# Optimization experiments

Measured on AMD Instinct MI355X. Metric: run time of the kernel, lower is better.

Reference implementation:

```python
import jax, jax.numpy as jnp
import numpy as np

EMD = 768
HEADS = 8
HEAD_DIM = EMD // HEADS


def setup_inputs() -> dict:
    key = jax.random.key(0)
    ks = jax.random.split(key, 9)
    s = 0.02
    x = jax.random.normal(ks[0], (4, 2048, EMD), dtype=jnp.float32)
    # torch nn.Linear weights: (out_features, in_features)
    Wq = jax.random.normal(ks[1], (EMD, EMD), dtype=jnp.float32) * s
    bq = jnp.zeros((EMD,), dtype=jnp.float32)
    Wk = jax.random.normal(ks[2], (EMD, EMD), dtype=jnp.float32) * s
    bk = jnp.zeros((EMD,), dtype=jnp.float32)
    Wv = jax.random.normal(ks[3], (EMD, EMD), dtype=jnp.float32) * s
    bv = jnp.zeros((EMD,), dtype=jnp.float32)
    Wo = jax.random.normal(ks[4], (EMD, EMD), dtype=jnp.float32) * s
    bo = jnp.zeros((EMD,), dtype=jnp.float32)
    return {"x": x, "Wq": Wq, "bq": bq, "Wk": Wk, "bk": bk,
            "Wv": Wv, "bv": bv, "Wo": Wo, "bo": bo}


def _split_heads(t):
    # [b, n, emd] -> [b, h, n, d]
    b, n, _ = t.shape
    return t.reshape(b, n, HEADS, HEAD_DIM).transpose(0, 2, 1, 3)


def reference(x, Wq, bq, Wk, bk, Wv, bv, Wo, bo):
    q = _split_heads(x @ Wq.T + bq)  # [b,h,n,d]
    k = _split_heads(x @ Wk.T + bk)
    v = _split_heads(x @ Wv.T + bv)
    energy = jnp.einsum('bhqd,bhkd->bhqk', q, k)  # [b,h,n,n]
    # NOTE: the original module applies softmax over the HEADS axis (dim=1),
    # then divides by sqrt(emd_size). We replicate that exactly.
    scaling = jnp.asarray(EMD ** 0.5, dtype=energy.dtype)
    attention = jax.nn.softmax(energy, axis=1) / scaling
    out = jnp.einsum('bhqk,bhkd->bhqd', attention, v)  # [b,h,n,d]
    b, h, n, d = out.shape
    out = out.transpose(0, 2, 1, 3).reshape(b, n, h * d)  # [b,n,emd]
    return out @ Wo.T + bo
```

## Files before the change

kernel.cpp:

```cpp
#include <hip/hip_runtime.h>
#include <stdint.h>

typedef __bf16 bf16;
typedef __bf16 bf16x4 __attribute__((ext_vector_type(4)));
typedef __bf16 bf16x8 __attribute__((ext_vector_type(8)));
typedef float  fx4    __attribute__((ext_vector_type(4)));

#define MFMA16(a, b, c) __builtin_amdgcn_mfma_f32_16x16x32_bf16((a), (b), (c), 0, 0, 0)


__device__ __forceinline__ void barrier_nodrain() {
  __asm__ __volatile__("" ::: "memory");
  __builtin_amdgcn_s_waitcnt(0xC07F);
  __builtin_amdgcn_s_barrier();
  __asm__ __volatile__("" ::: "memory");
}

__device__ __forceinline__ void wait_vm6() {
  __asm__ __volatile__("" ::: "memory");
  __builtin_amdgcn_s_waitcnt(0x0F76);
  __asm__ __volatile__("" ::: "memory");
}
__device__ __forceinline__ void wait_lgkm0() {
  __asm__ __volatile__("" ::: "memory");
  __builtin_amdgcn_s_waitcnt(0xC07F);
  __asm__ __volatile__("" ::: "memory");
}

__device__ __forceinline__ void gload_lds16(const void* g, void* l) {
  __builtin_amdgcn_global_load_lds(
      (const __attribute__((address_space(1))) void*)g,
      (__attribute__((address_space(3))) void*)l, 16, 0, 0);
}

__global__ __launch_bounds__(256)
void cvt_x_kernel(const float* __restrict__ x, bf16* __restrict__ xb) {
  const int i = (blockIdx.x * 256 + threadIdx.x) * 4;
  float4 v = *(const float4*)&x[i];
  bf16x4 o;
  o[0] = (bf16)v.x; o[1] = (bf16)v.y; o[2] = (bf16)v.z; o[3] = (bf16)v.w;
  *(bf16x4*)&xb[i] = o;
}

__global__ __launch_bounds__(256)
void gemm_qkv(const bf16* __restrict__ A,
              const float* __restrict__ Wq, const float* __restrict__ Wk,
              const float* __restrict__ Wv,
              const float* __restrict__ bq, const float* __restrict__ bk,
              const float* __restrict__ bv,
              bf16* __restrict__ Qo, bf16* __restrict__ Ka,
              bf16* __restrict__ Va) {
  constexpr int K = 768;
  __shared__ __align__(16) bf16 As[2][128 * 32];
  __shared__ __align__(16) bf16 Bs[128 * 32];

  const int tid  = threadIdx.x;
  const int wave = tid >> 6;
  const int lane = tid & 63;
  const int l15  = lane & 15;
  const int q4   = lane >> 4;
  const int wr   = wave >> 1;
  const int wc   = wave & 1;
  const int sel  = blockIdx.x / 6;
  const int cb0  = (blockIdx.x % 6) * 128;
  const int rb0  = blockIdx.y * 128;

  const float* W   = (sel == 0) ? Wq : (sel == 1) ? Wk : Wv;
  const float* bia = (sel == 0) ? bq : (sel == 1) ? bk : bv;

  const int ar0 = tid >> 2,         akc0 = (tid & 3) << 3;
  const int ar1 = ar0 + 64,         akc1 = akc0;

  fx4 acc[4][4];
#pragma unroll
  for (int i = 0; i < 4; i++)
#pragma unroll
    for (int j = 0; j < 4; j++) acc[i][j] = (fx4){0.f, 0.f, 0.f, 0.f};

  gload_lds16(&A[(size_t)(rb0 + ar0) * K + akc0], &As[0][wave * 512]);
  gload_lds16(&A[(size_t)(rb0 + ar1) * K + akc1], &As[0][(wave + 4) * 512]);

  int cur = 0;
  for (int k0 = 0; k0 < K; k0 += 32, cur ^= 1) {
    const float* wp0 = W + (size_t)(cb0 + ar0) * K + k0 + akc0;
    const float* wp1 = W + (size_t)(cb0 + ar1) * K + k0 + akc1;
    const float4 b0a = *(const float4*)wp0;
    const float4 b0b = *(const float4*)(wp0 + 4);
    const float4 b1a = *(const float4*)wp1;
    const float4 b1b = *(const float4*)(wp1 + 4);
    __asm__ __volatile__("" ::: "memory");

    const int kn = (k0 + 32 < K) ? k0 + 32 : k0;
    gload_lds16(&A[(size_t)(rb0 + ar0) * K + kn + akc0],
                &As[cur ^ 1][wave * 512]);
    gload_lds16(&A[(size_t)(rb0 + ar1) * K + kn + akc1],
                &As[cur ^ 1][(wave + 4) * 512]);
    __asm__ __volatile__("" ::: "memory");

    bf16x8 pb0, pb1;
    pb0[0] = (bf16)b0a.x; pb0[1] = (bf16)b0a.y;
    pb0[2] = (bf16)b0a.z; pb0[3] = (bf16)b0a.w;
    pb0[4] = (bf16)b0b.x; pb0[5] = (bf16)b0b.y;
    pb0[6] = (bf16)b0b.z; pb0[7] = (bf16)b0b.w;
    pb1[0] = (bf16)b1a.x; pb1[1] = (bf16)b1a.y;
    pb1[2] = (bf16)b1a.z; pb1[3] = (bf16)b1a.w;
    pb1[4] = (bf16)b1b.x; pb1[5] = (bf16)b1b.y;
    pb1[6] = (bf16)b1b.z; pb1[7] = (bf16)b1b.w;
    *(bf16x8*)&Bs[ar0 * 32 + akc0] = pb0;
    *(bf16x8*)&Bs[ar1 * 32 + akc1] = pb1;

    barrier_nodrain();

    bf16x8 a[4], b[4];
#pragma unroll
    for (int i = 0; i < 4; i++)
      a[i] = *(const bf16x8*)&As[cur][(wr * 64 + i * 16 + l15) * 32 + q4 * 8];
#pragma unroll
    for (int j = 0; j < 4; j++)
      b[j] = *(const bf16x8*)&Bs[(wc * 64 + j * 16 + l15) * 32 + q4 * 8];
#pragma unroll
    for (int i = 0; i < 4; i++)
#pragma unroll
      for (int j = 0; j < 4; j++)
        acc[i][j] = MFMA16(a[i], b[j], acc[i][j]);

    barrier_nodrain();
  }

  const int cb = cb0 + wc * 64;
  const int rb = rb0 + wr * 64;
#pragma unroll
  for (int j = 0; j < 4; j++) {
    const int o  = cb + j * 16 + l15;
    const float bj = bia[o];
    const int hh = o / 96;
    const int dd = o - hh * 96;
#pragma unroll
    for (int i = 0; i < 4; i++) {
      const int r0 = rb + i * 16 + q4 * 4;
      if (sel == 2) {
        const int bb = r0 >> 11;
        const int n2 = r0 & 2047;
        const size_t flat =
            ((size_t)((bb * 8 + hh) * 64 + (n2 >> 5))) * 3072 +
            ((n2 >> 3) & 3) * 768 + dd * 8 + (n2 & 7);
        bf16x4 pk;
#pragma unroll
        for (int r = 0; r < 4; r++) pk[r] = (bf16)(acc[i][j][r] + bj);
        *(bf16x4*)&Va[flat] = pk;
      } else if (sel == 1) {
        const int u  = dd >> 3;
        const int de = dd & 7;
#pragma unroll
        for (int r = 0; r < 4; r++) {
          const int n  = r0 + r;
          const int bb = n >> 11;
          const int n2 = n & 2047;
          const size_t flat =
              ((size_t)((bb * 8 + hh) * 64 + (n2 >> 5))) * 3072 +
              u * 256 + (n2 & 31) * 8 + de;
          Ka[flat] = (bf16)(acc[i][j][r] + bj);
        }
      } else {
#pragma unroll
        for (int r = 0; r < 4; r++)
          Qo[(size_t)(r0 + r) * 768 + o] = (bf16)(acc[i][j][r] + bj);
      }
    }
  }
}

__global__ __launch_bounds__(256)
void gemm_o(const bf16* __restrict__ A, const float* __restrict__ W,
            const float* __restrict__ bias, float* __restrict__ C) {
  constexpr int K = 768;
  __shared__ __align__(16) bf16 As[2][128 * 32];
  __shared__ __align__(16) bf16 Bs[128 * 32];

  const int tid  = threadIdx.x;
  const int wave = tid >> 6;
  const int lane = tid & 63;
  const int l15  = lane & 15;
  const int q4   = lane >> 4;
  const int wr   = wave >> 1;
  const int wc   = wave & 1;
  const int rb0  = blockIdx.y * 128;
  const int cb0  = blockIdx.x * 128;

  const int ar0 = tid >> 2,         akc0 = (tid & 3) << 3;
  const int ar1 = ar0 + 64,         akc1 = akc0;

  fx4 acc[4][4];
#pragma unroll
  for (int i = 0; i < 4; i++)
#pragma unroll
    for (int j = 0; j < 4; j++) acc[i][j] = (fx4){0.f, 0.f, 0.f, 0.f};

  gload_lds16(&A[(size_t)(rb0 + ar0) * K + akc0], &As[0][wave * 512]);
  gload_lds16(&A[(size_t)(rb0 + ar1) * K + akc1], &As[0][(wave + 4) * 512]);

  int cur = 0;
  for (int k0 = 0; k0 < K; k0 += 32, cur ^= 1) {
    const float* wp0 = W + (size_t)(cb0 + ar0) * K + k0 + akc0;
    const float* wp1 = W + (size_t)(cb0 + ar1) * K + k0 + akc1;
    const float4 b0a = *(const float4*)wp0;
    const float4 b0b = *(const float4*)(wp0 + 4);
    const float4 b1a = *(const float4*)wp1;
    const float4 b1b = *(const float4*)(wp1 + 4);
    __asm__ __volatile__("" ::: "memory");

    const int kn = (k0 + 32 < K) ? k0 + 32 : k0;
    gload_lds16(&A[(size_t)(rb0 + ar0) * K + kn + akc0],
                &As[cur ^ 1][wave * 512]);
    gload_lds16(&A[(size_t)(rb0 + ar1) * K + kn + akc1],
                &As[cur ^ 1][(wave + 4) * 512]);
    __asm__ __volatile__("" ::: "memory");

    bf16x8 pb0, pb1;
    pb0[0] = (bf16)b0a.x; pb0[1] = (bf16)b0a.y;
    pb0[2] = (bf16)b0a.z; pb0[3] = (bf16)b0a.w;
    pb0[4] = (bf16)b0b.x; pb0[5] = (bf16)b0b.y;
    pb0[6] = (bf16)b0b.z; pb0[7] = (bf16)b0b.w;
    pb1[0] = (bf16)b1a.x; pb1[1] = (bf16)b1a.y;
    pb1[2] = (bf16)b1a.z; pb1[3] = (bf16)b1a.w;
    pb1[4] = (bf16)b1b.x; pb1[5] = (bf16)b1b.y;
    pb1[6] = (bf16)b1b.z; pb1[7] = (bf16)b1b.w;
    *(bf16x8*)&Bs[ar0 * 32 + akc0] = pb0;
    *(bf16x8*)&Bs[ar1 * 32 + akc1] = pb1;

    barrier_nodrain();

    bf16x8 a[4], b[4];
#pragma unroll
    for (int i = 0; i < 4; i++)
      a[i] = *(const bf16x8*)&As[cur][(wr * 64 + i * 16 + l15) * 32 + q4 * 8];
#pragma unroll
    for (int j = 0; j < 4; j++)
      b[j] = *(const bf16x8*)&Bs[(wc * 64 + j * 16 + l15) * 32 + q4 * 8];
#pragma unroll
    for (int i = 0; i < 4; i++)
#pragma unroll
      for (int j = 0; j < 4; j++)
        acc[i][j] = MFMA16(a[i], b[j], acc[i][j]);

    barrier_nodrain();
  }

  const int cb = cb0 + wc * 64;
  const int rb = rb0 + wr * 64;
#pragma unroll
  for (int j = 0; j < 4; j++) {
    const int o  = cb + j * 16 + l15;
    const float bj = bias[o];
#pragma unroll
    for (int i = 0; i < 4; i++) {
      const int r0 = rb + i * 16 + q4 * 4;
#pragma unroll
      for (int r = 0; r < 4; r++)
        C[(size_t)(r0 + r) * 768 + o] = acc[i][j][r] + bj;
    }
  }
}

__global__ __launch_bounds__(512, 1)
void attn_kernel(const bf16* Q, const bf16* __restrict__ Ka,
                 const bf16* __restrict__ Va, bf16* AO) {
  __shared__ __align__(16) bf16  Kbuf[8 * 3072];
  __shared__ __align__(16) bf16  Vbuf[8 * 3072];
  __shared__ __align__(16) float Ebuf[32 * 260];

  const int tid  = threadIdx.x;
  const int h    = tid >> 6;
  const int lane = tid & 63;
  const int l15  = lane & 15;
  const int q4   = lane >> 4;
  const int b    = blockIdx.x >> 6;
  const int qt   = blockIdx.x & 63;
  const int qrow0 = b * 2048 + qt * 32;

  bf16x8 aq[2][3];
#pragma unroll
  for (int i = 0; i < 2; i++)
#pragma unroll
    for (int c = 0; c < 3; c++)
      aq[i][c] = *(const bf16x8*)
          &Q[(size_t)(qrow0 + i * 16 + l15) * 768 + h * 96 + c * 32 + q4 * 8];

  fx4 o[2][6];
#pragma unroll
  for (int i = 0; i < 2; i++)
#pragma unroll
    for (int j = 0; j < 6; j++) o[i][j] = (fx4){0.f, 0.f, 0.f, 0.f};

  const bf16* Kt0 = Ka + (size_t)(b * 8 + h) * 64 * 3072;
  const bf16* Vt0 = Va + (size_t)(b * 8 + h) * 64 * 3072;
  bf16* Kl = &Kbuf[h * 3072];
  bf16* Vl = &Vbuf[h * 3072];

  auto stageK = [&](int kt) {
    const bf16* src = Kt0 + (size_t)kt * 3072 + lane * 8;
#pragma unroll
    for (int t = 0; t < 6; t++)
      gload_lds16(src + t * 512, Kl + t * 512);
  };
  auto stageV = [&](int kt) {
    const bf16* src = Vt0 + (size_t)kt * 3072 + lane * 8;
#pragma unroll
    for (int t = 0; t < 6; t++)
      gload_lds16(src + t * 512, Vl + t * 512);
  };

  stageK(0);
  stageV(0);

  for (int kt = 0; kt < 64; kt++) {
    const int kn = (kt + 1 < 64) ? kt + 1 : 63;

    wait_vm6();

    bf16x8 bk[2][3];
#pragma unroll
    for (int j = 0; j < 2; j++)
#pragma unroll
      for (int c = 0; c < 3; c++)
        bk[j][c] =
            *(const bf16x8*)&Kl[(c * 4 + q4) * 256 + (j * 16 + l15) * 8];

    wait_lgkm0();
    stageK(kn);

    fx4 e[2][2];
    e[0][0] = e[0][1] = e[1][0] = e[1][1] = (fx4){0.f, 0.f, 0.f, 0.f};
#pragma unroll
    for (int c = 0; c < 3; c++)
#pragma unroll
      for (int j = 0; j < 2; j++) {
        e[0][j] = MFMA16(aq[0][c], bk[j][c], e[0][j]);
        e[1][j] = MFMA16(aq[1][c], bk[j][c], e[1][j]);
      }

#pragma unroll
    for (int i = 0; i < 2; i++)
#pragma unroll
      for (int j = 0; j < 2; j++)
#pragma unroll
        for (int r = 0; r < 4; r++)
          Ebuf[(i * 16 + q4 * 4 + r) * 260 + h * 32 + j * 16 + l15] =
              e[i][j][r];
    barrier_nodrain();

#pragma unroll
    for (int pp = 0; pp < 2; pp++) {
      const int p = tid + pp * 512;
      const int q = p >> 5, k = p & 31;
      float* row = &Ebuf[q * 260 + k];
      float v[8];
#pragma unroll
      for (int hh = 0; hh < 8; hh++) v[hh] = row[hh * 32];
      float m = v[0];
#pragma unroll
      for (int hh = 1; hh < 8; hh++) m = fmaxf(m, v[hh]);
      float sm = 0.f;
#pragma unroll
      for (int hh = 0; hh < 8; hh++) { v[hh] = __expf(v[hh] - m); sm += v[hh]; }
      const float inv = 1.0f / (sm * 27.712812921102035f);
#pragma unroll
      for (int hh = 0; hh < 8; hh++) row[hh * 32] = v[hh] * inv;
    }
    barrier_nodrain();

    wait_vm6();

    bf16x8 bv[6];
#pragma unroll
    for (int j2 = 0; j2 < 6; j2++)
      bv[j2] = *(const bf16x8*)&Vl[q4 * 768 + (j2 * 16 + l15) * 8];

    bf16x8 ap[2];
#pragma unroll
    for (int i = 0; i < 2; i++) {
      const float* ps = &Ebuf[(i * 16 + l15) * 260 + h * 32 + q4 * 8];
      fx4 p0 = *(const fx4*)ps;
      fx4 p1 = *(const fx4*)(ps + 4);
      bf16x8 t;
      t[0] = (bf16)p0[0]; t[1] = (bf16)p0[1];
      t[2] = (bf16)p0[2]; t[3] = (bf16)p0[3];
      t[4] = (bf16)p1[0]; t[5] = (bf16)p1[1];
      t[6] = (bf16)p1[2]; t[7] = (bf16)p1[3];
      ap[i] = t;
    }

    wait_lgkm0();
    stageV(kn);

#pragma unroll
    for (int j2 = 0; j2 < 6; j2++) {
      o[0][j2] = MFMA16(ap[0], bv[j2], o[0][j2]);
      o[1][j2] = MFMA16(ap[1], bv[j2], o[1][j2]);
    }
  }

  __builtin_amdgcn_s_waitcnt(0x0070);

#pragma unroll
  for (int i = 0; i < 2; i++)
#pragma unroll
    for (int j2 = 0; j2 < 6; j2++)
#pragma unroll
      for (int r = 0; r < 4; r++)
        AO[(size_t)(qrow0 + i * 16 + q4 * 4 + r) * 768 + h * 96 + j2 * 16 + l15] =
            (bf16)(o[i][j2][r]);
}

extern "C" void kernel_launch(void* const* d_in, const int* in_sizes, int n_in,
                              void* d_out, int out_size, void* d_ws,
                              size_t ws_size, hipStream_t stream) {
  const float* x  = (const float*)d_in[0];
  const float* Wq = (const float*)d_in[1];
  const float* bq = (const float*)d_in[2];
  const float* Wk = (const float*)d_in[3];
  const float* bk = (const float*)d_in[4];
  const float* Wv = (const float*)d_in[5];
  const float* bv = (const float*)d_in[6];
  const float* Wo = (const float*)d_in[7];
  const float* bo = (const float*)d_in[8];

  const size_t MN = (size_t)8192 * 768;
  bf16* xb = (bf16*)d_out;
  bf16* Ka = xb + MN;
  bf16* Q  = (bf16*)d_ws;
  bf16* Va = Q + MN;
  bf16* AO = Q;

  cvt_x_kernel<<<6144, 256, 0, stream>>>(x, xb);
  dim3 qkvgrid(18, 64);
  gemm_qkv<<<qkvgrid, 256, 0, stream>>>(xb, Wq, Wk, Wv, bq, bk, bv, Q, Ka, Va);
  attn_kernel<<<256, 512, 0, stream>>>(Q, Ka, Va, AO);
  dim3 ogrid(6, 64);
  gemm_o<<<ogrid, 256, 0, stream>>>(AO, Wo, bo, (float*)d_out);
}
```

Baseline: 316.4 us.

## Transpose QK MFMA, vectorize softmax over two keys, stage bf16 probs buffer

```diff
diff --git a/kernel.cpp b/kernel.cpp
--- a/kernel.cpp
+++ b/kernel.cpp
@@ -2,8 +2,10 @@
 #include <stdint.h>
 
 typedef __bf16 bf16;
+typedef __bf16 bf16x2 __attribute__((ext_vector_type(2)));
 typedef __bf16 bf16x4 __attribute__((ext_vector_type(4)));
 typedef __bf16 bf16x8 __attribute__((ext_vector_type(8)));
+typedef float  fx2    __attribute__((ext_vector_type(2)));
 typedef float  fx4    __attribute__((ext_vector_type(4)));
 
 #define MFMA16(a, b, c) __builtin_amdgcn_mfma_f32_16x16x32_bf16((a), (b), (c), 0, 0, 0)
@@ -268,6 +270,7 @@
   __shared__ __align__(16) bf16  Kbuf[8 * 3072];
   __shared__ __align__(16) bf16  Vbuf[8 * 3072];
   __shared__ __align__(16) float Ebuf[32 * 260];
+  __shared__ __align__(16) bf16  Pbuf[8 * 32 * 40];
 
   const int tid  = threadIdx.x;
   const int h    = tid >> 6;
@@ -329,43 +332,55 @@
     wait_lgkm0();
     stageK(kn);
 
-    fx4 e[2][2];
-    e[0][0] = e[0][1] = e[1][0] = e[1][1] = (fx4){0.f, 0.f, 0.f, 0.f};
+    fx4 e2[2][2];
+    e2[0][0] = e2[0][1] = e2[1][0] = e2[1][1] = (fx4){0.f, 0.f, 0.f, 0.f};
+    __builtin_amdgcn_s_setprio(1);
 #pragma unroll
     for (int c = 0; c < 3; c++)
 #pragma unroll
       for (int j = 0; j < 2; j++) {
-        e[0][j] = MFMA16(aq[0][c], bk[j][c], e[0][j]);
-        e[1][j] = MFMA16(aq[1][c], bk[j][c], e[1][j]);
+        e2[j][0] = MFMA16(bk[j][c], aq[0][c], e2[j][0]);
+        e2[j][1] = MFMA16(bk[j][c], aq[1][c], e2[j][1]);
       }
+    __builtin_amdgcn_s_setprio(0);
 
 #pragma unroll
     for (int i = 0; i < 2; i++)
 #pragma unroll
       for (int j = 0; j < 2; j++)
-#pragma unroll
-        for (int r = 0; r < 4; r++)
-          Ebuf[(i * 16 + q4 * 4 + r) * 260 + h * 32 + j * 16 + l15] =
-              e[i][j][r];
-    barrier_nodrain();
-
-#pragma unroll
-    for (int pp = 0; pp < 2; pp++) {
-      const int p = tid + pp * 512;
-      const int q = p >> 5, k = p & 31;
-      float* row = &Ebuf[q * 260 + k];
-      float v[8];
-#pragma unroll
-      for (int hh = 0; hh < 8; hh++) v[hh] = row[hh * 32];
-      float m = v[0];
-#pragma unroll
-      for (int hh = 1; hh < 8; hh++) m = fmaxf(m, v[hh]);
-      float sm = 0.f;
-#pragma unroll
-      for (int hh = 0; hh < 8; hh++) { v[hh] = __expf(v[hh] - m); sm += v[hh]; }
-      const float inv = 1.0f / (sm * 27.712812921102035f);
-#pragma unroll
-      for (int hh = 0; hh < 8; hh++) row[hh * 32] = v[hh] * inv;
+        *(fx4*)&Ebuf[(i * 16 + l15) * 260 + h * 32 + j * 16 + q4 * 4] =
+            e2[j][i];
+    barrier_nodrain();
+
+    {
+      const int q  = tid >> 4;
+      const int k2 = (tid & 15) << 1;
+      const float* row = &Ebuf[q * 260 + k2];
+      fx2 v[8];
+#pragma unroll
+      for (int hh = 0; hh < 8; hh++) v[hh] = *(const fx2*)&row[hh * 32];
+      fx2 m = v[0];
+#pragma unroll
+      for (int hh = 1; hh < 8; hh++) {
+        m[0] = fmaxf(m[0], v[hh][0]);
+        m[1] = fmaxf(m[1], v[hh][1]);
+      }
+      fx2 sm = (fx2){0.f, 0.f};
+#pragma unroll
+      for (int hh = 0; hh < 8; hh++) {
+        v[hh][0] = __expf(v[hh][0] - m[0]);
+        v[hh][1] = __expf(v[hh][1] - m[1]);
+        sm += v[hh];
+      }
+      const float inv0 = 1.0f / (sm[0] * 27.712812921102035f);
+      const float inv1 = 1.0f / (sm[1] * 27.712812921102035f);
+#pragma unroll
+      for (int hh = 0; hh < 8; hh++) {
+        bf16x2 pk;
+        pk[0] = (bf16)(v[hh][0] * inv0);
+        pk[1] = (bf16)(v[hh][1] * inv1);
+        *(bf16x2*)&Pbuf[hh * 1280 + q * 40 + k2] = pk;
+      }
     }
     barrier_nodrain();
 
@@ -378,26 +393,19 @@
 
     bf16x8 ap[2];
 #pragma unroll
-    for (int i = 0; i < 2; i++) {
-      const float* ps = &Ebuf[(i * 16 + l15) * 260 + h * 32 + q4 * 8];
-      fx4 p0 = *(const fx4*)ps;
-      fx4 p1 = *(const fx4*)(ps + 4);
-      bf16x8 t;
-      t[0] = (bf16)p0[0]; t[1] = (bf16)p0[1];
-      t[2] = (bf16)p0[2]; t[3] = (bf16)p0[3];
-      t[4] = (bf16)p1[0]; t[5] = (bf16)p1[1];
-      t[6] = (bf16)p1[2]; t[7] = (bf16)p1[3];
-      ap[i] = t;
-    }
+    for (int i = 0; i < 2; i++)
+      ap[i] = *(const bf16x8*)&Pbuf[h * 1280 + (i * 16 + l15) * 40 + q4 * 8];
 
     wait_lgkm0();
     stageV(kn);
 
+    __builtin_amdgcn_s_setprio(1);
 #pragma unroll
     for (int j2 = 0; j2 < 6; j2++) {
       o[0][j2] = MFMA16(ap[0], bv[j2], o[0][j2]);
       o[1][j2] = MFMA16(ap[1], bv[j2], o[1][j2]);
     }
+    __builtin_amdgcn_s_setprio(0);
   }
 
   __builtin_amdgcn_s_waitcnt(0x0070);
```

Measured after the change: 313.9 us. No clear change (-0.8%).

## Halve attention tiles to 16x16 and double block count for occupancy

Applied to the files above, without the earlier changes.

```diff
diff --git a/kernel.cpp b/kernel.cpp
--- a/kernel.cpp
+++ b/kernel.cpp
@@ -2,8 +2,10 @@
 #include <stdint.h>
 
 typedef __bf16 bf16;
+typedef __bf16 bf16x2 __attribute__((ext_vector_type(2)));
 typedef __bf16 bf16x4 __attribute__((ext_vector_type(4)));
 typedef __bf16 bf16x8 __attribute__((ext_vector_type(8)));
+typedef float  fx2    __attribute__((ext_vector_type(2)));
 typedef float  fx4    __attribute__((ext_vector_type(4)));
 
 #define MFMA16(a, b, c) __builtin_amdgcn_mfma_f32_16x16x32_bf16((a), (b), (c), 0, 0, 0)
@@ -16,9 +18,9 @@
   __asm__ __volatile__("" ::: "memory");
 }
 
-__device__ __forceinline__ void wait_vm6() {
-  __asm__ __volatile__("" ::: "memory");
-  __builtin_amdgcn_s_waitcnt(0x0F76);
+__device__ __forceinline__ void wait_vm3() {
+  __asm__ __volatile__("" ::: "memory");
+  __builtin_amdgcn_s_waitcnt(0x0F73);
   __asm__ __volatile__("" ::: "memory");
 }
 __device__ __forceinline__ void wait_lgkm0() {
@@ -142,8 +144,8 @@
         const int bb = r0 >> 11;
         const int n2 = r0 & 2047;
         const size_t flat =
-            ((size_t)((bb * 8 + hh) * 64 + (n2 >> 5))) * 3072 +
-            ((n2 >> 3) & 3) * 768 + dd * 8 + (n2 & 7);
+            ((size_t)((bb * 8 + hh) * 128 + (n2 >> 4))) * 1536 +
+            ((n2 >> 3) & 1) * 768 + dd * 8 + (n2 & 7);
         bf16x4 pk;
 #pragma unroll
         for (int r = 0; r < 4; r++) pk[r] = (bf16)(acc[i][j][r] + bj);
@@ -157,8 +159,8 @@
           const int bb = n >> 11;
           const int n2 = n & 2047;
           const size_t flat =
-              ((size_t)((bb * 8 + hh) * 64 + (n2 >> 5))) * 3072 +
-              u * 256 + (n2 & 31) * 8 + de;
+              ((size_t)((bb * 8 + hh) * 128 + (n2 >> 4))) * 1536 +
+              u * 128 + (n2 & 15) * 8 + de;
           Ka[flat] = (bf16)(acc[i][j][r] + bj);
         }
       } else {
@@ -262,101 +264,84 @@
   }
 }
 
-__global__ __launch_bounds__(512, 1)
+__global__ __launch_bounds__(512, 2)
 void attn_kernel(const bf16* Q, const bf16* __restrict__ Ka,
                  const bf16* __restrict__ Va, bf16* AO) {
-  __shared__ __align__(16) bf16  Kbuf[8 * 3072];
-  __shared__ __align__(16) bf16  Vbuf[8 * 3072];
-  __shared__ __align__(16) float Ebuf[32 * 260];
+  __shared__ __align__(16) bf16  Kbuf[8 * 1536];
+  __shared__ __align__(16) bf16  Vbuf[8 * 1536];
+  __shared__ __align__(16) float Ebuf[16 * 132];
+  __shared__ __align__(16) bf16  Pbuf[8 * 16 * 24];
 
   const int tid  = threadIdx.x;
   const int h    = tid >> 6;
   const int lane = tid & 63;
   const int l15  = lane & 15;
   const int q4   = lane >> 4;
-  const int b    = blockIdx.x >> 6;
-  const int qt   = blockIdx.x & 63;
-  const int qrow0 = b * 2048 + qt * 32;
-
-  bf16x8 aq[2][3];
-#pragma unroll
-  for (int i = 0; i < 2; i++)
-#pragma unroll
-    for (int c = 0; c < 3; c++)
-      aq[i][c] = *(const bf16x8*)
-          &Q[(size_t)(qrow0 + i * 16 + l15) * 768 + h * 96 + c * 32 + q4 * 8];
-
-  fx4 o[2][6];
-#pragma unroll
-  for (int i = 0; i < 2; i++)
-#pragma unroll
-    for (int j = 0; j < 6; j++) o[i][j] = (fx4){0.f, 0.f, 0.f, 0.f};
-
-  const bf16* Kt0 = Ka + (size_t)(b * 8 + h) * 64 * 3072;
-  const bf16* Vt0 = Va + (size_t)(b * 8 + h) * 64 * 3072;
-  bf16* Kl = &Kbuf[h * 3072];
-  bf16* Vl = &Vbuf[h * 3072];
+  const int bid  = blockIdx.x;
+  const int b    = (bid & 7) >> 1;
+  const int qt   = ((bid & 1) << 6) | (bid >> 3);
+  const int qrow0 = b * 2048 + qt * 16;
+
+  bf16x8 aq[3];
+#pragma unroll
+  for (int c = 0; c < 3; c++)
+    aq[c] = *(const bf16x8*)
+        &Q[(size_t)(qrow0 + l15) * 768 + h * 96 + c * 32 + q4 * 8];
+
+  fx4 o[6];
+#pragma unroll
+  for (int j = 0; j < 6; j++) o[j] = (fx4){0.f, 0.f, 0.f, 0.f};
+
+  const bf16* Kt0 = Ka + (size_t)(b * 8 + h) * 128 * 1536;
+  const bf16* Vt0 = Va + (size_t)(b * 8 + h) * 128 * 1536;
+  bf16* Kl = &Kbuf[h * 1536];
+  bf16* Vl = &Vbuf[h * 1536];
 
   auto stageK = [&](int kt) {
-    const bf16* src = Kt0 + (size_t)kt * 3072 + lane * 8;
-#pragma unroll
-    for (int t = 0; t < 6; t++)
+    const bf16* src = Kt0 + (size_t)kt * 1536 + lane * 8;
+#pragma unroll
+    for (int t = 0; t < 3; t++)
       gload_lds16(src + t * 512, Kl + t * 512);
   };
   auto stageV = [&](int kt) {
-    const bf16* src = Vt0 + (size_t)kt * 3072 + lane * 8;
-#pragma unroll
-    for (int t = 0; t < 6; t++)
+    const bf16* src = Vt0 + (size_t)kt * 1536 + lane * 8;
+#pragma unroll
+    for (int t = 0; t < 3; t++)
       gload_lds16(src + t * 512, Vl + t * 512);
   };
 
   stageK(0);
   stageV(0);
 
-  for (int kt = 0; kt < 64; kt++) {
-    const int kn = (kt + 1 < 64) ? kt + 1 : 63;
-
-    wait_vm6();
-
-    bf16x8 bk[2][3];
-#pragma unroll
-    for (int j = 0; j < 2; j++)
-#pragma unroll
-      for (int c = 0; c < 3; c++)
-        bk[j][c] =
-            *(const bf16x8*)&Kl[(c * 4 + q4) * 256 + (j * 16 + l15) * 8];
+  for (int kt = 0; kt < 128; kt++) {
+    const int kn = (kt + 1 < 128) ? kt + 1 : 127;
+
+    wait_vm3();
+
+    bf16x8 bk[3];
+#pragma unroll
+    for (int c = 0; c < 3; c++)
+      bk[c] = *(const bf16x8*)&Kl[(c * 4 + q4) * 128 + l15 * 8];
 
     wait_lgkm0();
     stageK(kn);
 
-    fx4 e[2][2];
-    e[0][0] = e[0][1] = e[1][0] = e[1][1] = (fx4){0.f, 0.f, 0.f, 0.f};
+    fx4 e2 = (fx4){0.f, 0.f, 0.f, 0.f};
+    __builtin_amdgcn_s_setprio(1);
 #pragma unroll
     for (int c = 0; c < 3; c++)
-#pragma unroll
-      for (int j = 0; j < 2; j++) {
-        e[0][j] = MFMA16(aq[0][c], bk[j][c], e[0][j]);
-        e[1][j] = MFMA16(aq[1][c], bk[j][c], e[1][j]);
-      }
-
-#pragma unroll
-    for (int i = 0; i < 2; i++)
-#pragma unroll
-      for (int j = 0; j < 2; j++)
-#pragma unroll
-        for (int r = 0; r < 4; r++)
-          Ebuf[(i * 16 + q4 * 4 + r) * 260 + h * 32 + j * 16 + l15] =
-              e[i][j][r];
-    barrier_nodrain();
-
-#pragma unroll
-    for (int pp = 0; pp < 2; pp++) {
-      const int p = tid + pp * 512;
-      const int q = p >> 5, k = p & 31;
-      float* row = &Ebuf[q * 260 + k];
+      e2 = MFMA16(bk[c], aq[c], e2);
+    __builtin_amdgcn_s_setprio(0);
+
+    *(fx4*)&Ebuf[l15 * 132 + h * 16 + q4 * 4] = e2;
+    barrier_nodrain();
+
+    if (tid < 256) {
+      const int q = tid & 15, k = tid >> 4;
+      const float* row = &Ebuf[q * 132 + k];
       float v[8];
 #pragma unroll
-      for (int hh = 0; hh < 8; hh++) v[hh] = row[hh * 32];
+      for (int hh = 0; hh < 8; hh++) v[hh] = row[hh * 16];
       float m = v[0];
 #pragma unroll
       for (int hh = 1; hh < 8; hh++) m = fmaxf(m, v[hh]);
@@ -365,51 +350,46 @@
       for (int hh = 0; hh < 8; hh++) { v[hh] = __expf(v[hh] - m); sm += v[hh]; }
       const float inv = 1.0f / (sm * 27.712812921102035f);
 #pragma unroll
-      for (int hh = 0; hh < 8; hh++) row[hh * 32] = v[hh] * inv;
+      for (int hh = 0; hh < 8; hh++)
+        Pbuf[hh * 384 + q * 24 + k] = (bf16)(v[hh] * inv);
     }
     barrier_nodrain();
 
-    wait_vm6();
-
-    bf16x8 bv[6];
-#pragma unroll
-    for (int j2 = 0; j2 < 6; j2++)
-      bv[j2] = *(const bf16x8*)&Vl[q4 * 768 + (j2 * 16 + l15) * 8];
-
-    bf16x8 ap[2];
-#pragma unroll
-    for (int i = 0; i < 2; i++) {
-      const float* ps = &Ebuf[(i * 16 + l15) * 260 + h * 32 + q4 * 8];
-      fx4 p0 = *(const fx4*)ps;
-      fx4 p1 = *(const fx4*)(ps + 4);
-      bf16x8 t;
-      t[0] = (bf16)p0[0]; t[1] = (bf16)p0[1];
-      t[2] = (bf16)p0[2]; t[3] = (bf16)p0[3];
-      t[4] = (bf16)p1[0]; t[5] = (bf16)p1[1];
-      t[6] = (bf16)p1[2]; t[7] = (bf16)p1[3];
-      ap[i] = t;
+    wait_vm3();
+
+    bf16x8 bv[6], ap;
+    if (q4 < 2) {
+#pragma unroll
+      for (int j2 = 0; j2 < 6; j2++)
+        bv[j2] = *(const bf16x8*)&Vl[q4 * 768 + (j2 * 16 + l15) * 8];
+      ap = *(const bf16x8*)&Pbuf[h * 384 + l15 * 24 + q4 * 8];
+    } else {
+      bf16x8 z;
+#pragma unroll
+      for (int t = 0; t < 8; t++) z[t] = (bf16)0.f;
+#pragma unroll
+      for (int j2 = 0; j2 < 6; j2++) bv[j2] = z;
+      ap = z;
     }
 
     wait_lgkm0();
     stageV(kn);
 
-#pragma unroll
-    for (int j2 = 0; j2 < 6; j2++) {
-      o[0][j2] = MFMA16(ap[0], bv[j2], o[0][j2]);
-      o[1][j2] = MFMA16(ap[1], bv[j2], o[1][j2]);
-    }
+    __builtin_amdgcn_s_setprio(1);
+#pragma unroll
+    for (int j2 = 0; j2 < 6; j2++)
+      o[j2] = MFMA16(ap, bv[j2], o[j2]);
+    __builtin_amdgcn_s_setprio(0);
   }
 
   __builtin_amdgcn_s_waitcnt(0x0070);
 
 #pragma unroll
-  for (int i = 0; i < 2; i++)
-#pragma unroll
-    for (int j2 = 0; j2 < 6; j2++)
-#pragma unroll
-      for (int r = 0; r < 4; r++)
-        AO[(size_t)(qrow0 + i * 16 + q4 * 4 + r) * 768 + h * 96 + j2 * 16 + l15] =
-            (bf16)(o[i][j2][r]);
+  for (int j2 = 0; j2 < 6; j2++)
+#pragma unroll
+    for (int r = 0; r < 4; r++)
+      AO[(size_t)(qrow0 + q4 * 4 + r) * 768 + h * 96 + j2 * 16 + l15] =
+          (bf16)(o[j2][r]);
 }
 
 extern "C" void kernel_launch(void* const* d_in, const int* in_sizes, int n_in,
@@ -435,7 +415,7 @@
   cvt_x_kernel<<<6144, 256, 0, stream>>>(x, xb);
   dim3 qkvgrid(18, 64);
   gemm_qkv<<<qkvgrid, 256, 0, stream>>>(xb, Wq, Wk, Wv, bq, bk, bv, Q, Ka, Va);
-  attn_kernel<<<256, 512, 0, stream>>>(Q, Ka, Va, AO);
+  attn_kernel<<<512, 512, 0, stream>>>(Q, Ka, Va, AO);
   dim3 ogrid(6, 64);
   gemm_o<<<ogrid, 256, 0, stream>>>(AO, Wo, bo, (float*)d_out);
 }
```

New measurement: 391.8 us. 1.24x slower.
